# Performance work log

Hardware: AMD Instinct MI355X
Metric: run time of the kernel (lower is better)

Reference implementation:

```python
import jax, jax.numpy as jnp
import numpy as np

N, E, DIN, H, DOUT = 50000, 1600000, 16, 256, 2
EPS = 1e-5


def _glorot(key, shape):
    fan_in = shape[0]
    return jax.random.normal(key, shape, dtype=jnp.float32) * (1.0 / np.sqrt(fan_in))


def setup_inputs() -> dict:
    key = jax.random.key(0)
    ks = jax.random.split(key, 16)
    x = jax.random.normal(ks[0], (N, DIN), dtype=jnp.float32)
    edge_index = jax.random.randint(ks[1], (2, E), 0, N, dtype=jnp.int64)
    edge_weight = jax.random.uniform(ks[2], (E,), dtype=jnp.float32)
    return {
        "x": x,
        "edge_index": edge_index,
        "edge_weight": edge_weight,
        # GCN layer 1 and 2
        "W1": _glorot(ks[3], (DIN, H)), "b1": jnp.zeros((H,), jnp.float32),
        "g1": jnp.ones((H,), jnp.float32), "be1": jnp.zeros((H,), jnp.float32),
        "W2": _glorot(ks[4], (H, H)), "b2": jnp.zeros((H,), jnp.float32),
        "g2": jnp.ones((H,), jnp.float32), "be2": jnp.zeros((H,), jnp.float32),
        # GRU (single layer): weight_ih [3H, H], weight_hh [3H, H]
        "Wih": _glorot(ks[5], (H, 3 * H)).T * 0.5,
        "Whh": _glorot(ks[6], (H, 3 * H)).T * 0.5,
        "bih": jnp.zeros((3 * H,), jnp.float32),
        "bhh": jnp.zeros((3 * H,), jnp.float32),
        # decoder MLP
        "Wd1": _glorot(ks[7], (H + DIN, H)), "bd1": jnp.zeros((H,), jnp.float32),
        "Wd2": _glorot(ks[8], (H, H // 2)), "bd2": jnp.zeros((H // 2,), jnp.float32),
        "Wd3": _glorot(ks[9], (H // 2, DOUT)), "bd3": jnp.zeros((DOUT,), jnp.float32),
    }


def _gcn_conv(x, W, b, src, dst, ew, n):
    # GCNConv(improved=True): A_hat = A + 2I, sym-normalized, messages aggregated at dst
    xw = x @ W  # [n, H]
    sl = jnp.arange(n, dtype=src.dtype)
    src_f = jnp.concatenate([src, sl])
    dst_f = jnp.concatenate([dst, sl])
    ew_f = jnp.concatenate([ew, jnp.full((n,), 2.0, ew.dtype)])
    deg = jax.ops.segment_sum(ew_f, dst_f, num_segments=n)
    dis = jnp.where(deg > 0, jax.lax.rsqrt(jnp.maximum(deg, 1e-12)), 0.0)
    norm = dis[src_f] * ew_f * dis[dst_f]  # [E+n]
    out = jax.ops.segment_sum(xw[src_f] * norm[:, None], dst_f, num_segments=n)
    return out + b


def _layernorm(h, g, be):
    mu = jnp.mean(h, axis=-1, keepdims=True)
    var = jnp.mean(jnp.square(h - mu), axis=-1, keepdims=True)
    return (h - mu) * jax.lax.rsqrt(var + EPS) * g + be


def _gru_step(x, h, Wih, Whh, bih, bhh):
    gi = x @ Wih.T + bih  # [n, 3H]
    gh = h @ Whh.T + bhh
    i_r, i_z, i_n = jnp.split(gi, 3, axis=-1)
    h_r, h_z, h_n = jnp.split(gh, 3, axis=-1)
    r = jax.nn.sigmoid(i_r + h_r)
    z = jax.nn.sigmoid(i_z + h_z)
    n = jnp.tanh(i_n + r * h_n)
    return (1.0 - z) * n + z * h


def reference(x, edge_index, edge_weight, W1, b1, g1, be1, W2, b2, g2, be2,
              Wih, Whh, bih, bhh, Wd1, bd1, Wd2, bd2, Wd3, bd3):
    n = x.shape[0]
    src, dst = edge_index[0], edge_index[1]
    # spatial encoding (eval mode: dropout off)
    h = _gcn_conv(x, W1, b1, src, dst, edge_weight, n)
    h = jax.nn.relu(_layernorm(h, g1, be1))
    h = _gcn_conv(h, W2, b2, src, dst, edge_weight, n)
    h = _layernorm(h, g2, be2)  # last layer: no relu
    # GRU single timestep, zero initial hidden state per agent
    h0 = jnp.zeros_like(h)
    temporal = _gru_step(h, h0, Wih, Whh, bih, bhh)
    # decoder MLP on [temporal, x]
    d = jnp.concatenate([temporal, x], axis=-1)
    d = jax.nn.relu(d @ Wd1 + bd1)
    d = jax.nn.relu(d @ Wd2 + bd2)
    pred = d @ Wd3 + bd3
    return jnp.clip(pred, -5.0, 5.0)
```

## Files before the change

kernel.cpp:

```cpp
#include <hip/hip_runtime.h>
#include <math.h>

#define N_NODES 50000
#define N_EDGES 1600000
#define DIN 16
#define H 256
#define RPB 16
#define LN_EPS 1e-5f
#define FIXS 8388608.0f
#define NB 391
#define CAP 5120
#define TILEA 4096
#define NTILES 391
#define GRU_COLS 48
#define GRU_STR 272
#define DSTR 264

typedef __attribute__((ext_vector_type(8))) unsigned short u16x8;
typedef __attribute__((ext_vector_type(8))) __bf16 bf16x8;
typedef __attribute__((ext_vector_type(4))) float f32x4;

__device__ inline unsigned short f2bf(float f) {
    unsigned u = __builtin_bit_cast(unsigned, f);
    return (unsigned short)((u + 0x7FFFu + ((u >> 16) & 1u)) >> 16);
}
__device__ inline float bf2f(unsigned short u) {
    return __builtin_bit_cast(float, ((unsigned)u) << 16);
}
__device__ inline float fsig(float x) { return 1.0f / (1.0f + __expf(-x)); }
__device__ inline float ftanh(float x) { return 2.0f / (1.0f + __expf(-2.0f * x)) - 1.0f; }

__global__ void k_wprep(const float* Wih, const float* W2, const float* Wd1, const float* Wd2,
                        const float* x, unsigned short* Wg, unsigned short* W2T,
                        unsigned short* Wd1T, unsigned short* Wd2T, unsigned short* xb,
                        int* bcursor) {
    int idx = blockIdx.x * blockDim.x + threadIdx.x;
    if (idx < 768 * 256) { Wg[idx] = f2bf(Wih[idx]); return; }
    idx -= 768 * 256;
    if (idx < 256 * 256) { int k = idx >> 8, n = idx & 255; W2T[n * 256 + k] = f2bf(W2[idx]); return; }
    idx -= 256 * 256;
    if (idx < 256 * 288) {
        int n = idx / 288, k = idx % 288;
        Wd1T[idx] = (k < 272) ? f2bf(Wd1[k * 256 + n]) : (unsigned short)0;
        return;
    }
    idx -= 256 * 288;
    if (idx < 128 * 256) { int k = idx >> 7, n = idx & 127; Wd2T[n * 256 + k] = f2bf(Wd2[idx]); return; }
    idx -= 128 * 256;
    if (idx < N_NODES * 32) {
        int row = idx >> 5, j = idx & 31;
        xb[idx] = (j < 16) ? f2bf(x[row * DIN + j]) : (unsigned short)0;
        return;
    }
    idx -= N_NODES * 32;
    if (idx < 512) bcursor[idx] = 0;
}

__global__ __launch_bounds__(256) void k_msplit(const void* ei, const float* ew,
                                                int* bcursor, unsigned long long* stage) {
    __shared__ int bh[512], bscn[512], cur[512], gbase[512];
    __shared__ int ws4[4];
    __shared__ unsigned long long sdata[TILEA];
    __shared__ unsigned short sbkt[TILEA];
    int t = threadIdx.x;
    long long base = (long long)blockIdx.x * TILEA;
    int nhere = (int)(((long long)N_EDGES - base) < TILEA ? (N_EDGES - base) : TILEA);
    for (int i = t; i < 512; i += 256) bh[i] = 0;
    bool f64;
    {
        const long long* p = (const long long*)ei;
        f64 = true;
        for (int i = 0; i < 8; ++i) { long long v = p[i]; if (v < 0 || v >= N_NODES) f64 = false; }
    }
    __syncthreads();
    unsigned long long vreg[TILEA / 256];
    int breg[TILEA / 256];
#pragma unroll
    for (int k = 0; k < TILEA / 256; ++k) {
        long long e = base + k * 256 + t;
        if (e < N_EDGES) {
            int s, d;
            if (f64) {
                const long long* p = (const long long*)ei;
                s = (int)p[e]; d = (int)p[N_EDGES + e];
            } else {
                const int* p = (const int*)ei;
                s = p[e]; d = p[N_EDGES + e];
            }
            unsigned wbits = __builtin_bit_cast(unsigned, ew[e]);
            vreg[k] = ((unsigned long long)wbits << 32) |
                      ((unsigned long long)(d & 127) << 16) | (unsigned)(s & 0xFFFF);
            breg[k] = d >> 7;
            atomicAdd(&bh[breg[k]], 1);
        } else breg[k] = -1;
    }
    __syncthreads();
    int a0 = bh[2 * t], a1 = bh[2 * t + 1];
    int s = a0 + a1;
    int lane = t & 63, wv = t >> 6;
    int sc = s;
    for (int d = 1; d < 64; d <<= 1) { int u = __shfl_up(sc, d, 64); if (lane >= d) sc += u; }
    if (lane == 63) ws4[wv] = sc;
    __syncthreads();
    int wpre = 0;
    for (int i = 0; i < wv; ++i) wpre += ws4[i];
    int excl = wpre + sc - s;
    bscn[2 * t] = excl;      cur[2 * t] = excl;
    bscn[2 * t + 1] = excl + a0; cur[2 * t + 1] = excl + a0;
    __syncthreads();
    for (int i = t; i < NB; i += 256) {
        int c = bh[i];
        if (c) gbase[i] = atomicAdd(&bcursor[i], c);
    }
    __syncthreads();
#pragma unroll
    for (int k = 0; k < TILEA / 256; ++k) {
        if (breg[k] >= 0) {
            int p = atomicAdd(&cur[breg[k]], 1);
            sdata[p] = vreg[k];
            sbkt[p] = (unsigned short)breg[k];
        }
    }
    __syncthreads();
    for (int i = t; i < nhere; i += 256) {
        int b = sbkt[i];
        stage[(long long)b * CAP + gbase[b] + (i - bscn[b])] = sdata[i];
    }
}

__global__ __launch_bounds__(256) void k_bfin(const unsigned long long* __restrict__ stage,
                                              const int* __restrict__ bcursor,
                                              const float* __restrict__ x,
                                              float* __restrict__ dis,
                                              int* __restrict__ offs, int* __restrict__ oend,
                                              unsigned* __restrict__ csr,
                                              unsigned short* __restrict__ xpb) {
    __shared__ unsigned long long acc[128];
    __shared__ int sc[128];
    __shared__ int cur[128];
    __shared__ float sdis[128];
    int b = blockIdx.x, t = threadIdx.x;
    if (t < 128) acc[t] = 0ULL;
    __syncthreads();
    long long e0 = (long long)b * CAP;
    int n = bcursor[b];
    for (int i = t; i < n; i += 256) {
        unsigned long long v = stage[e0 + i];
        int nl = (int)((v >> 16) & 127);
        float w = __builtin_bit_cast(float, (unsigned)(v >> 32));
        atomicAdd(&acc[nl], (1ULL << 43) | (unsigned long long)llrintf(w * FIXS));
    }
    __syncthreads();
    int mycnt = 0;
    if (t < 128) {
        unsigned long long v = acc[t];
        mycnt = (int)(v >> 43);
        sc[t] = mycnt;
        float dv = rsqrtf((float)(v & ((1ULL << 43) - 1)) * (1.0f / FIXS) + 2.0f);
        sdis[t] = dv;
        int node = (b << 7) + t;
        if (node < N_NODES) dis[node] = dv;
    }
    __syncthreads();
    for (int d = 1; d < 128; d <<= 1) {
        int v = 0;
        if (t < 128 && t >= d) v = sc[t - d];
        __syncthreads();
        if (t < 128 && t >= d) sc[t] += v;
        __syncthreads();
    }
    if (t < 128) {
        int excl = sc[t] - mycnt;
        cur[t] = excl;
        int node = (b << 7) + t;
        if (node < N_NODES) {
            offs[node] = (int)(e0 + excl);
            oend[node] = (int)(e0 + excl + mycnt);
        }
    }
    __syncthreads();
    for (int i = t; i < n; i += 256) {
        unsigned long long v = stage[e0 + i];
        int nl = (int)((v >> 16) & 127);
        int p = atomicAdd(&cur[nl], 1);
        float w = __builtin_bit_cast(float, (unsigned)(v >> 32));
        csr[e0 + p] = ((unsigned)f2bf(w) << 16) | (unsigned)(v & 0xFFFFu);
    }
    for (int i = t; i < 128 * DIN; i += 256) {
        int nl = i >> 4, dd = i & 15;
        int node = (b << 7) + nl;
        if (node < N_NODES) xpb[node * DIN + dd] = f2bf(sdis[nl] * x[node * DIN + dd]);
    }
}

__global__ __launch_bounds__(256) void k_l1(const unsigned short* __restrict__ xpb,
        const int* __restrict__ offs, const int* __restrict__ oend,
        const unsigned* __restrict__ csr, const float* __restrict__ dis,
        const float* __restrict__ W, const float* __restrict__ bias,
        const float* __restrict__ g, const float* __restrict__ be,
        unsigned short* __restrict__ out) {
    __shared__ float s[RPB][H + 1];
    __shared__ float smu[RPB], srs[RPB];
    int t = threadIdx.x;
    long long rowbase = (long long)blockIdx.x * RPB;
    {
        int r = blockIdx.x * 16 + (t >> 4);
        int dd = t & 15;
        float di = dis[r];
        float xself = bf2f(xpb[(long long)r * DIN + dd]);
        float acc = 0.0f;
        int e0 = offs[r], e1 = oend[r];
        for (int e = e0; e < e1; e += 8) {
            unsigned vv[8];
#pragma unroll
            for (int j = 0; j < 8; ++j) {
                int idx = e + j;
                vv[j] = (idx < e1) ? csr[idx] : (unsigned)r;
            }
            float xx[8];
#pragma unroll
            for (int j = 0; j < 8; ++j) {
                int sidx = (int)(vv[j] & 0xFFFFu);
                xx[j] = bf2f(xpb[(long long)sidx * DIN + dd]);
            }
#pragma unroll
            for (int j = 0; j < 8; ++j) {
                float c = bf2f((unsigned short)(vv[j] >> 16));
                acc = fmaf(c, xx[j], acc);
            }
        }
        s[t >> 4][dd] = di * acc + 2.0f * di * xself;
    }
    __syncthreads();
    float acc2[RPB];
    float bb0 = bias[t];
#pragma unroll
    for (int r = 0; r < RPB; ++r) acc2[r] = bb0;
    for (int k = 0; k < DIN; ++k) {
        float wv = W[k * H + t];
#pragma unroll
        for (int r = 0; r < RPB; ++r) acc2[r] = fmaf(s[r][k], wv, acc2[r]);
    }
    __syncthreads();
#pragma unroll
    for (int r = 0; r < RPB; ++r) s[r][t] = acc2[r];
    __syncthreads();
    int lane = t & 63, wv2 = t >> 6;
    for (int rr = wv2; rr < RPB; rr += 4) {
        float v0 = s[rr][lane], v1 = s[rr][lane + 64], v2 = s[rr][lane + 128], v3 = s[rr][lane + 192];
        float sm = v0 + v1 + v2 + v3;
        float sq = v0 * v0 + v1 * v1 + v2 * v2 + v3 * v3;
        for (int d = 32; d; d >>= 1) {
            sm += __shfl_down(sm, d, 64);
            sq += __shfl_down(sq, d, 64);
        }
        if (lane == 0) {
            float mu = sm * (1.0f / H);
            float var = sq * (1.0f / H) - mu * mu;
            smu[rr] = mu;
            srs[rr] = rsqrtf(var + LN_EPS);
        }
    }
    __syncthreads();
    float gg = g[t], bb = be[t];
#pragma unroll
    for (int r = 0; r < RPB; ++r) {
        float h = fmaxf((acc2[r] - smu[r]) * srs[r] * gg + bb, 0.0f);
        out[(rowbase + r) * H + t] = f2bf(h * dis[rowbase + r]);
    }
}

__global__ __launch_bounds__(256) void k_spmm(const unsigned short* __restrict__ hin,
                                              unsigned short* __restrict__ hout,
                                              const int* __restrict__ offs,
                                              const int* __restrict__ oend,
                                              const unsigned* __restrict__ csr,
                                              const float* __restrict__ dis) {
    int t = threadIdx.x;
    int wv = t >> 6, lane = t & 63;
    int row = blockIdx.x * 4 + wv;
    const ushort4* h4 = (const ushort4*)hin;
    float di = dis[row];
    ushort4 vs = h4[(long long)row * 64 + lane];
    float a0 = 0.f, a1 = 0.f, a2 = 0.f, a3 = 0.f;
    int e0 = offs[row], e1 = oend[row];
    for (int e = e0; e < e1; e += 16) {
        unsigned vv[16];
#pragma unroll
        for (int j = 0; j < 16; ++j) {
            int idx = e + j;
            vv[j] = (idx < e1) ? csr[idx] : (unsigned)row;
        }
        ushort4 uu[16];
#pragma unroll
        for (int j = 0; j < 16; ++j) {
            int s = (int)(vv[j] & 0xFFFFu);
            uu[j] = h4[(long long)s * 64 + lane];
        }
#pragma unroll
        for (int j = 0; j < 16; ++j) {
            float c = bf2f((unsigned short)(vv[j] >> 16));
            a0 = fmaf(c, bf2f(uu[j].x), a0);
            a1 = fmaf(c, bf2f(uu[j].y), a1);
            a2 = fmaf(c, bf2f(uu[j].z), a2);
            a3 = fmaf(c, bf2f(uu[j].w), a3);
        }
    }
    ushort4 o;
    o.x = f2bf(di * a0 + 2.0f * di * bf2f(vs.x));
    o.y = f2bf(di * a1 + 2.0f * di * bf2f(vs.y));
    o.z = f2bf(di * a2 + 2.0f * di * bf2f(vs.z));
    o.w = f2bf(di * a3 + 2.0f * di * bf2f(vs.w));
    ((ushort4*)hout)[(long long)row * 64 + lane] = o;
}

__global__ __launch_bounds__(256) void k_lgd(
        const unsigned short* __restrict__ Bbf,
        const unsigned short* __restrict__ W2T, const float* __restrict__ b2,
        const float* __restrict__ g2, const float* __restrict__ be2,
        const unsigned short* __restrict__ Wg, const float* __restrict__ bih,
        const float* __restrict__ bhh,
        const unsigned short* __restrict__ W1T, const float* __restrict__ bd1,
        const unsigned short* __restrict__ Wd2T, const float* __restrict__ bd2,
        const float* __restrict__ Wd3, const float* __restrict__ bd3,
        const unsigned short* __restrict__ xb, float* __restrict__ out) {
    __shared__ unsigned short wbuf[GRU_COLS * GRU_STR];
    __shared__ unsigned short dtile[64][DSTR];
    int t = threadIdx.x;
    int wv = t >> 6, l = t & 63;
    int lr = l & 15, lg = l >> 4;
    int rb = blockIdx.x * 64 + wv * 16;
    int arow = rb + lr; if (arow >= N_NODES) arow = N_NODES - 1;

    {
        bf16x8 af[8];
        const unsigned short* ap = Bbf + (long long)arow * H + lg * 8;
#pragma unroll
        for (int ks = 0; ks < 8; ++ks) af[ks] = __builtin_bit_cast(bf16x8, *(const u16x8*)(ap + ks * 32));
        f32x4 acc[16];
#pragma unroll
        for (int ct = 0; ct < 16; ++ct) acc[ct] = (f32x4){0.f, 0.f, 0.f, 0.f};
        for (int ct = 0; ct < 16; ++ct) {
            const unsigned short* wr = W2T + (ct * 16 + lr) * H + lg * 8;
#pragma unroll
            for (int ks = 0; ks < 8; ++ks) {
                bf16x8 bfv = __builtin_bit_cast(bf16x8, *(const u16x8*)(wr + ks * 32));
                acc[ct] = __builtin_amdgcn_mfma_f32_16x16x32_bf16(af[ks], bfv, acc[ct], 0, 0, 0);
            }
        }
#pragma unroll
        for (int ct = 0; ct < 16; ++ct) {
            float bb = b2[ct * 16 + lr];
#pragma unroll
            for (int q = 0; q < 4; ++q) acc[ct][q] += bb;
        }
        float mean[4], rstd[4];
#pragma unroll
        for (int q = 0; q < 4; ++q) {
            float s = 0.f, s2 = 0.f;
#pragma unroll
            for (int ct = 0; ct < 16; ++ct) { float v = acc[ct][q]; s += v; s2 += v * v; }
#pragma unroll
            for (int m = 1; m < 16; m <<= 1) { s += __shfl_xor(s, m, 64); s2 += __shfl_xor(s2, m, 64); }
            float mu = s * (1.0f / H);
            mean[q] = mu;
            rstd[q] = rsqrtf(s2 * (1.0f / H) - mu * mu + LN_EPS);
        }
#pragma unroll
        for (int ct = 0; ct < 16; ++ct) {
            int col = ct * 16 + lr;
            float gg = g2[col], bb = be2[col];
#pragma unroll
            for (int q = 0; q < 4; ++q) {
                float nv = (acc[ct][q] - mean[q]) * rstd[q] * gg + bb;
                dtile[wv * 16 + lg * 4 + q][col] = f2bf(nv);
            }
        }
    }
    __syncthreads();

    {
        bf16x8 ah[8];
        const unsigned short* lp = &dtile[wv * 16 + lr][0] + lg * 8;
#pragma unroll
        for (int ks = 0; ks < 8; ++ks) ah[ks] = __builtin_bit_cast(bf16x8, *(const u16x8*)(lp + ks * 32));
        for (int ct = 0; ct < 16; ++ct) {
#pragma unroll
            for (int j = 0; j < 6; ++j) {
                int i = t + j * 256;
                int col = i >> 5;
                int off = (i & 31) * 8;
                int gate = col >> 4, c = col & 15;
                u16x8 v = *(const u16x8*)(Wg + ((gate * 256 + ct * 16 + c) * 256 + off));
                *(u16x8*)(&wbuf[col * GRU_STR + off]) = v;
            }
            __syncthreads();
            f32x4 aR = (f32x4){0.f, 0.f, 0.f, 0.f};
            f32x4 aZ = aR, aN = aR;
            const unsigned short* base = wbuf + lr * GRU_STR + lg * 8;
#pragma unroll
            for (int ks = 0; ks < 8; ++ks) {
                bf16x8 b0 = __builtin_bit_cast(bf16x8, *(const u16x8*)(base + ks * 32));
                bf16x8 b1 = __builtin_bit_cast(bf16x8, *(const u16x8*)(base + 16 * GRU_STR + ks * 32));
                bf16x8 b2v = __builtin_bit_cast(bf16x8, *(const u16x8*)(base + 32 * GRU_STR + ks * 32));
                aR = __builtin_amdgcn_mfma_f32_16x16x32_bf16(ah[ks], b0, aR, 0, 0, 0);
                aZ = __builtin_amdgcn_mfma_f32_16x16x32_bf16(ah[ks], b1, aZ, 0, 0, 0);
                aN = __builtin_amdgcn_mfma_f32_16x16x32_bf16(ah[ks], b2v, aN, 0, 0, 0);
            }
            int col = ct * 16 + lr;
            float bR = bih[col] + bhh[col];
            float bZ = bih[col + 256] + bhh[col + 256];
            float bN = bih[col + 512];
            float hN = bhh[col + 512];
#pragma unroll
            for (int q = 0; q < 4; ++q) {
                float r = fsig(aR[q] + bR);
                float z = fsig(aZ[q] + bZ);
                float nn = ftanh(aN[q] + bN + r * hN);
                dtile[wv * 16 + lg * 4 + q][col] = f2bf((1.0f - z) * nn);
            }
            __syncthreads();
        }
    }

    {
        bf16x8 ad[9];
        const unsigned short* lp = &dtile[wv * 16 + lr][0] + lg * 8;
#pragma unroll
        for (int ks = 0; ks < 8; ++ks) ad[ks] = __builtin_bit_cast(bf16x8, *(const u16x8*)(lp + ks * 32));
        ad[8] = __builtin_bit_cast(bf16x8, *(const u16x8*)(xb + (long long)arow * 32 + lg * 8));
        __syncthreads();
        f32x4 acc[16];
#pragma unroll
        for (int ct = 0; ct < 16; ++ct) acc[ct] = (f32x4){0.f, 0.f, 0.f, 0.f};
        for (int ct = 0; ct < 16; ++ct) {
            const unsigned short* wr = W1T + (ct * 16 + lr) * 288 + lg * 8;
#pragma unroll
            for (int ks = 0; ks < 9; ++ks) {
                bf16x8 bfv = __builtin_bit_cast(bf16x8, *(const u16x8*)(wr + ks * 32));
                acc[ct] = __builtin_amdgcn_mfma_f32_16x16x32_bf16(ad[ks], bfv, acc[ct], 0, 0, 0);
            }
        }
#pragma unroll
        for (int ct = 0; ct < 16; ++ct) {
            float bb = bd1[ct * 16 + lr];
#pragma unroll
            for (int q = 0; q < 4; ++q) {
                float v = fmaxf(acc[ct][q] + bb, 0.0f);
                dtile[wv * 16 + lg * 4 + q][ct * 16 + lr] = f2bf(v);
            }
        }
    }
    __syncthreads();

    bf16x8 af[8];
    const unsigned short* lp = &dtile[wv * 16 + lr][0] + lg * 8;
#pragma unroll
    for (int ks = 0; ks < 8; ++ks) af[ks] = __builtin_bit_cast(bf16x8, *(const u16x8*)(lp + ks * 32));
    f32x4 acc[8];
#pragma unroll
    for (int ct = 0; ct < 8; ++ct) acc[ct] = (f32x4){0.f, 0.f, 0.f, 0.f};
    for (int ct = 0; ct < 8; ++ct) {
        const unsigned short* wr = Wd2T + (ct * 16 + lr) * H + lg * 8;
#pragma unroll
        for (int ks = 0; ks < 8; ++ks) {
            bf16x8 bfv = __builtin_bit_cast(bf16x8, *(const u16x8*)(wr + ks * 32));
            acc[ct] = __builtin_amdgcn_mfma_f32_16x16x32_bf16(af[ks], bfv, acc[ct], 0, 0, 0);
        }
    }
    float p0[4] = {0.f, 0.f, 0.f, 0.f}, p1[4] = {0.f, 0.f, 0.f, 0.f};
#pragma unroll
    for (int ct = 0; ct < 8; ++ct) {
        int col = ct * 16 + lr;
        float bb = bd2[col];
        float2 w3 = *(const float2*)(Wd3 + col * 2);
#pragma unroll
        for (int q = 0; q < 4; ++q) {
            float v = fmaxf(acc[ct][q] + bb, 0.0f);
            p0[q] = fmaf(v, w3.x, p0[q]);
            p1[q] = fmaf(v, w3.y, p1[q]);
        }
    }
#pragma unroll
    for (int q = 0; q < 4; ++q) {
#pragma unroll
        for (int m = 1; m < 16; m <<= 1) {
            p0[q] += __shfl_xor(p0[q], m, 64);
            p1[q] += __shfl_xor(p1[q], m, 64);
        }
    }
    if (lr == 0) {
#pragma unroll
        for (int q = 0; q < 4; ++q) {
            int row = rb + lg * 4 + q;
            if (row < N_NODES) {
                float a = fminf(fmaxf(p0[q] + bd3[0], -5.0f), 5.0f);
                float b = fminf(fmaxf(p1[q] + bd3[1], -5.0f), 5.0f);
                out[(long long)row * 2] = a;
                out[(long long)row * 2 + 1] = b;
            }
        }
    }
}

extern "C" void kernel_launch(void* const* d_in, const int* in_sizes, int n_in,
                              void* d_out, int out_size, void* d_ws, size_t ws_size,
                              hipStream_t stream) {
    const float* x   = (const float*)d_in[0];
    const void*  ei  = d_in[1];
    const float* ew  = (const float*)d_in[2];
    const float* W1  = (const float*)d_in[3];
    const float* b1  = (const float*)d_in[4];
    const float* g1  = (const float*)d_in[5];
    const float* be1 = (const float*)d_in[6];
    const float* W2  = (const float*)d_in[7];
    const float* b2  = (const float*)d_in[8];
    const float* g2  = (const float*)d_in[9];
    const float* be2 = (const float*)d_in[10];
    const float* Wih = (const float*)d_in[11];
    const float* bih = (const float*)d_in[13];
    const float* bhh = (const float*)d_in[14];
    const float* Wd1 = (const float*)d_in[15];
    const float* bd1 = (const float*)d_in[16];
    const float* Wd2 = (const float*)d_in[17];
    const float* bd2 = (const float*)d_in[18];
    const float* Wd3 = (const float*)d_in[19];
    const float* bd3 = (const float*)d_in[20];
    float* out = (float*)d_out;

    char* w = (char*)d_ws;
    size_t pos = 0;
    auto carve = [&](size_t bytes) -> void* {
        void* p = w + pos;
        pos += (bytes + 255) & ~(size_t)255;
        return p;
    };
    int*   bcursor = (int*)carve(sizeof(int) * 512);
    float* dis     = (float*)carve(sizeof(float) * N_NODES);
    int*   offs    = (int*)carve(sizeof(int) * N_NODES);
    int*   oend    = (int*)carve(sizeof(int) * N_NODES);
    unsigned long long* stage = (unsigned long long*)carve(8 * (size_t)NB * CAP);
    unsigned* csr = (unsigned*)carve(4 * (size_t)NB * CAP);
    unsigned short* xpb  = (unsigned short*)carve(2 * (size_t)N_NODES * DIN);
    unsigned short* xb   = (unsigned short*)carve(2 * (size_t)N_NODES * 32);
    unsigned short* Wg   = (unsigned short*)carve(2 * 768 * 256);
    unsigned short* W2T  = (unsigned short*)carve(2 * 256 * 256);
    unsigned short* Wd1T = (unsigned short*)carve(2 * 256 * 288);
    unsigned short* Wd2T = (unsigned short*)carve(2 * 128 * 256);
    unsigned short* Abf = (unsigned short*)carve(2 * (size_t)N_NODES * H);
    unsigned short* Bbf = (unsigned short*)carve(2 * (size_t)N_NODES * H);
    (void)pos; (void)ws_size; (void)in_sizes; (void)n_in; (void)out_size;

    int nbm = (N_NODES + 63) / 64;
    int nwp = (768 * 256 + 256 * 256 + 256 * 288 + 128 * 256 + N_NODES * 32 + 512 + 255) / 256;

    k_wprep<<<nwp, 256, 0, stream>>>(Wih, W2, Wd1, Wd2, x, Wg, W2T, Wd1T, Wd2T, xb, bcursor);
    k_msplit<<<NTILES, 256, 0, stream>>>(ei, ew, bcursor, stage);
    k_bfin<<<NB, 256, 0, stream>>>(stage, bcursor, x, dis, offs, oend, csr, xpb);
    k_l1<<<N_NODES / RPB, 256, 0, stream>>>(xpb, offs, oend, csr, dis, W1, b1, g1, be1, Abf);
    k_spmm<<<N_NODES / 4, 256, 0, stream>>>(Abf, Bbf, offs, oend, csr, dis);
    k_lgd<<<nbm, 256, 0, stream>>>(Bbf, W2T, b2, g2, be2, Wg, bih, bhh,
                                   Wd1T, bd1, Wd2T, bd2, Wd3, bd3, xb, out);
}
```

Before: 389.3 us.

## Double-buffer GRU weight staging per gate to overlap loads with MFMA

The GRU stage in k_lgd now splits each 48-column weight tile into three 16-column gate slices held in a two-slot LDS buffer. The next slice is staged while MFMAs run on the current one, which replaces the load-then-sync-then-compute pattern. The aim is to hide global weight-load latency and cut LDS footprint so occupancy can rise. The cost is three times as many barriers (48 instead of 32) and less MFMA work between each sync.

```diff
diff --git a/kernel.cpp b/kernel.cpp
--- a/kernel.cpp
+++ b/kernel.cpp
@@ -12,7 +12,6 @@
 #define CAP 5120
 #define TILEA 4096
 #define NTILES 391
-#define GRU_COLS 48
 #define GRU_STR 272
 #define DSTR 264
 
@@ -324,7 +323,7 @@
         const unsigned short* __restrict__ Wd2T, const float* __restrict__ bd2,
         const float* __restrict__ Wd3, const float* __restrict__ bd3,
         const unsigned short* __restrict__ xb, float* __restrict__ out) {
-    __shared__ unsigned short wbuf[GRU_COLS * GRU_STR];
+    __shared__ unsigned short wbuf[2][16 * GRU_STR];
     __shared__ unsigned short dtile[64][DSTR];
     int t = threadIdx.x;
     int wv = t >> 6, l = t & 63;
@@ -384,41 +383,49 @@
         const unsigned short* lp = &dtile[wv * 16 + lr][0] + lg * 8;
 #pragma unroll
         for (int ks = 0; ks < 8; ++ks) ah[ks] = __builtin_bit_cast(bf16x8, *(const u16x8*)(lp + ks * 32));
-        for (int ct = 0; ct < 16; ++ct) {
-#pragma unroll
-            for (int j = 0; j < 6; ++j) {
+        auto stageg = [&](int ctS, int gateS, int b) {
+#pragma unroll
+            for (int j = 0; j < 2; ++j) {
                 int i = t + j * 256;
                 int col = i >> 5;
                 int off = (i & 31) * 8;
-                int gate = col >> 4, c = col & 15;
-                u16x8 v = *(const u16x8*)(Wg + ((gate * 256 + ct * 16 + c) * 256 + off));
-                *(u16x8*)(&wbuf[col * GRU_STR + off]) = v;
-            }
-            __syncthreads();
-            f32x4 aR = (f32x4){0.f, 0.f, 0.f, 0.f};
-            f32x4 aZ = aR, aN = aR;
-            const unsigned short* base = wbuf + lr * GRU_STR + lg * 8;
+                u16x8 v = *(const u16x8*)(Wg + ((gateS * 256 + ctS * 16 + col) * 256 + off));
+                *(u16x8*)(&wbuf[b][col * GRU_STR + off]) = v;
+            }
+        };
+        stageg(0, 0, 0);
+        __syncthreads();
+        f32x4 ag0, ag1, ag2;
+        int ct = 0, gate = 0;
+        for (int s = 0; s < 48; ++s) {
+            int gate_n = (gate == 2) ? 0 : gate + 1;
+            int ct_n = (gate == 2) ? ct + 1 : ct;
+            if (s < 47) stageg(ct_n, gate_n, (s + 1) & 1);
+            const unsigned short* base = &wbuf[s & 1][0] + lr * GRU_STR + lg * 8;
+            f32x4 a = (f32x4){0.f, 0.f, 0.f, 0.f};
 #pragma unroll
             for (int ks = 0; ks < 8; ++ks) {
-                bf16x8 b0 = __builtin_bit_cast(bf16x8, *(const u16x8*)(base + ks * 32));
-                bf16x8 b1 = __builtin_bit_cast(bf16x8, *(const u16x8*)(base + 16 * GRU_STR + ks * 32));
-                bf16x8 b2v = __builtin_bit_cast(bf16x8, *(const u16x8*)(base + 32 * GRU_STR + ks * 32));
-                aR = __builtin_amdgcn_mfma_f32_16x16x32_bf16(ah[ks], b0, aR, 0, 0, 0);
-                aZ = __builtin_amdgcn_mfma_f32_16x16x32_bf16(ah[ks], b1, aZ, 0, 0, 0);
-                aN = __builtin_amdgcn_mfma_f32_16x16x32_bf16(ah[ks], b2v, aN, 0, 0, 0);
-            }
-            int col = ct * 16 + lr;
-            float bR = bih[col] + bhh[col];
-            float bZ = bih[col + 256] + bhh[col + 256];
-            float bN = bih[col + 512];
-            float hN = bhh[col + 512];
-#pragma unroll
-            for (int q = 0; q < 4; ++q) {
-                float r = fsig(aR[q] + bR);
-                float z = fsig(aZ[q] + bZ);
-                float nn = ftanh(aN[q] + bN + r * hN);
-                dtile[wv * 16 + lg * 4 + q][col] = f2bf((1.0f - z) * nn);
-            }
+                bf16x8 bv = __builtin_bit_cast(bf16x8, *(const u16x8*)(base + ks * 32));
+                a = __builtin_amdgcn_mfma_f32_16x16x32_bf16(ah[ks], bv, a, 0, 0, 0);
+            }
+            if (gate == 0) ag0 = a;
+            else if (gate == 1) ag1 = a;
+            else ag2 = a;
+            if (gate == 2) {
+                int col = ct * 16 + lr;
+                float bR = bih[col] + bhh[col];
+                float bZ = bih[col + 256] + bhh[col + 256];
+                float bN = bih[col + 512];
+                float hN = bhh[col + 512];
+#pragma unroll
+                for (int q = 0; q < 4; ++q) {
+                    float r = fsig(ag0[q] + bR);
+                    float z = fsig(ag1[q] + bZ);
+                    float nn = ftanh(ag2[q] + bN + r * hN);
+                    dtile[wv * 16 + lg * 4 + q][col] = f2bf((1.0f - z) * nn);
+                }
+            }
+            ct = ct_n; gate = gate_n;
             __syncthreads();
         }
     }
```

Result: slower. 432.2 us (+11.0%).
